# Performance work log

Hardware: AMD Instinct MI355X
Metric: run time of the kernel (lower is better)

## Reference

```python
import jax, jax.numpy as jnp
import numpy as np

N_POINTS = 2097152
FEAT_DIM = 32
RES = [256, 256, 256, 128]  # xyzt resolutions
COO_COMBS = [[0, 3], [1, 3], [2, 3]]
INIT_A, INIT_B = 0.1, 0.5


def _bilinear_sample(plane, cx, cy):
    """F.grid_sample(align_corners=True, padding_mode='border') for one plane.

    plane: [F, H, W]; cx, cy: [N] normalized coords in [-1, 1].
    Returns [N, F].
    """
    Fd, H, W = plane.shape
    # unnormalize (align_corners=True) then border-clamp the coordinate itself
    x = jnp.clip((cx + 1.0) * 0.5 * (W - 1), 0.0, W - 1)
    y = jnp.clip((cy + 1.0) * 0.5 * (H - 1), 0.0, H - 1)
    x0 = jnp.floor(x)
    y0 = jnp.floor(y)
    wx = (x - x0)[:, None]
    wy = (y - y0)[:, None]
    x0i = x0.astype(jnp.int32)
    y0i = y0.astype(jnp.int32)
    x1i = jnp.minimum(x0i + 1, W - 1)
    y1i = jnp.minimum(y0i + 1, H - 1)
    p = jnp.transpose(plane, (1, 2, 0))  # [H, W, F] for gather
    v00 = p[y0i, x0i]  # [N, F]
    v01 = p[y0i, x1i]
    v10 = p[y1i, x0i]
    v11 = p[y1i, x1i]
    return (v00 * (1 - wx) * (1 - wy) + v01 * wx * (1 - wy)
            + v10 * (1 - wx) * wy + v11 * wx * wy)


def setup_inputs() -> dict:
    key = jax.random.key(0)
    k_inp, k0, k1, k2 = jax.random.split(key, 4)
    inp = jax.random.uniform(k_inp, (N_POINTS, 4), dtype=jnp.float32,
                             minval=-1.0, maxval=1.0)
    planes = {}
    for name, k, comb in (("plane0", k0, COO_COMBS[0]),
                          ("plane1", k1, COO_COMBS[1]),
                          ("plane2", k2, COO_COMBS[2])):
        shape = (FEAT_DIM, RES[comb[1]], RES[comb[0]])
        planes[name] = jax.random.uniform(k, shape, dtype=jnp.float32,
                                          minval=INIT_A, maxval=INIT_B)
    return {"inp": inp, **planes}


def reference(inp, plane0, plane1, plane2):
    # reduce='sum': sum of three bilinear plane lookups
    out = 0.0
    for plane, comb in zip((plane0, plane1, plane2), COO_COMBS):
        out = out + _bilinear_sample(plane, inp[..., comb[0]], inp[..., comb[1]])
    return out  # [N, FEAT_DIM]
```

## Files before the change

kernel.cpp:

```cpp
#include <hip/hip_runtime.h>
#include <hip/hip_fp16.h>


#define NPTS 2097152
#define FEAT 32
#define PW 256
#define PH 128
#define NBINS 128
#define BIN_CAP 24576
#define NCHUNKS 4

__global__ __launch_bounds__(128) void zero_counts_kernel(int* counts) {
    counts[threadIdx.x] = 0;
}

__global__ __launch_bounds__(1024) void scatter_kernel(
    const float* __restrict__ inp,
    float4* __restrict__ s_pts,
    int* __restrict__ counts) {
    __shared__ int hist[NBINS];
    __shared__ int base[NBINS];
    int tid = threadIdx.x;
    if (tid < NBINS) hist[tid] = 0;
    __syncthreads();

    float4 c[8];
    int tag[8];
    unsigned int pw[8];
    int p0 = blockIdx.x * 8192 + tid;
#pragma unroll
    for (int i = 0; i < 8; ++i) {
        c[i] = reinterpret_cast<const float4*>(inp)[p0 + i * 1024];
        float y = fminf(fmaxf((c[i].w + 1.0f) * 63.5f, 0.0f), 127.0f);
        float bf = floorf(y);
        int bin = (int)bf;
        int wyq = (int)((y - bf) * 2048.0f);
        pw[i] = ((unsigned int)(p0 + i * 1024) << 11) | (unsigned int)wyq;
        int lpos = atomicAdd(&hist[bin], 1);
        tag[i] = (bin << 16) | lpos;
    }
    __syncthreads();
    if (tid < NBINS) base[tid] = atomicAdd(&counts[tid], hist[tid]);
    __syncthreads();
#pragma unroll
    for (int i = 0; i < 8; ++i) {
        int bin = tag[i] >> 16;
        int pos = base[bin] + (tag[i] & 0xffff);
        s_pts[bin * BIN_CAP + pos] =
            make_float4(c[i].x, c[i].y, c[i].z, __uint_as_float(pw[i]));
    }
}

__device__ __forceinline__ unsigned int pk16(float a, float b) {
    __half2 h = __floats2half2_rn(a, b);
    return *reinterpret_cast<unsigned int*>(&h);
}
__device__ __forceinline__ float2 up16(unsigned int u) {
    __half2 h = *reinterpret_cast<__half2*>(&u);
    return __half22float2(h);
}

__global__ __launch_bounds__(1024) void sample_lds_kernel(
    const float* __restrict__ pl0,
    const float* __restrict__ pl1,
    const float* __restrict__ pl2,
    const float4* __restrict__ s_pts,
    const int* __restrict__ counts,
    float* __restrict__ out) {
    __shared__ uint4 tex[6 * PW * 4];
    __shared__ float bounce[FEAT * PW];

    const int chunk = blockIdx.x;
    const int bin = blockIdx.y;
    const int tid = threadIdx.x;
    const int r1 = min(bin + 1, PH - 1);
    const float* planes[3] = {pl0, pl1, pl2};

    for (int i = 0; i < 6; ++i) {
        const float* src = planes[i >> 1] + ((i & 1) ? r1 : bin) * PW;
        {
            int f = tid >> 6;
            int x4 = (tid & 63) << 2;
            float4 a = *reinterpret_cast<const float4*>(src + f * (PH * PW) + x4);
            float4 b = *reinterpret_cast<const float4*>(src + (f + 16) * (PH * PW) + x4);
            *reinterpret_cast<float4*>(bounce + f * PW + x4) = a;
            *reinterpret_cast<float4*>(bounce + (f + 16) * PW + x4) = b;
        }
        __syncthreads();
        {
            int slot = tid >> 8;
            int x = tid & 255;
            const float* bp = bounce + (slot << 3) * PW + x;
            uint4 v;
            v.x = pk16(bp[0],      bp[PW]);
            v.y = pk16(bp[2 * PW], bp[3 * PW]);
            v.z = pk16(bp[4 * PW], bp[5 * PW]);
            v.w = pk16(bp[6 * PW], bp[7 * PW]);
            int swz = (slot + ((x >> 1) & 3)) & 3;
            tex[(i << 10) | (x << 2) | swz] = v;
        }
        __syncthreads();
    }

    const int cnt = min(counts[bin], BIN_CAP);
    const int pid = tid >> 2;
    const int f4 = tid & 3;

    for (int s0 = chunk * 256; s0 < cnt; s0 += NCHUNKS * 256) {
        int slot = s0 + pid;
        if (slot < cnt) {
            float4 c = s_pts[bin * BIN_CAP + slot];
            unsigned int pw = __float_as_uint(c.w);
            int id = pw >> 11;
            float wy = (float)(pw & 2047u) * (1.0f / 2048.0f);
            float omy = 1.0f - wy;

            float a0 = 0, a1 = 0, a2 = 0, a3 = 0, a4 = 0, a5 = 0, a6 = 0, a7 = 0;
            const float cx[3] = {c.x, c.y, c.z};
#pragma unroll
            for (int k = 0; k < 3; ++k) {
                float x = fminf(fmaxf((cx[k] + 1.0f) * 127.5f, 0.0f), 255.0f);
                float x0f = floorf(x);
                float wx = x - x0f;
                float omx = 1.0f - wx;
                int x0 = (int)x0f;
                int x1 = min(x0 + 1, PW - 1);
                float w00 = omx * omy, w01 = wx * omy;
                float w10 = omx * wy, w11 = wx * wy;

                int b0 = (k * 2) << 10;
                int b1 = b0 + 1024;
                int i0 = (x0 << 2) | ((f4 + ((x0 >> 1) & 3)) & 3);
                int i1 = (x1 << 2) | ((f4 + ((x1 >> 1) & 3)) & 3);
                uint4 t00 = tex[b0 | i0];
                uint4 t01 = tex[b0 | i1];
                uint4 t10 = tex[b1 | i0];
                uint4 t11 = tex[b1 | i1];
#define ACC(T, W) { float2 u0 = up16(T.x), u1 = up16(T.y), u2 = up16(T.z), u3 = up16(T.w); \
                a0 += u0.x * W; a1 += u0.y * W; a2 += u1.x * W; a3 += u1.y * W; \
                a4 += u2.x * W; a5 += u2.y * W; a6 += u3.x * W; a7 += u3.y * W; }
                ACC(t00, w00) ACC(t01, w01) ACC(t10, w10) ACC(t11, w11)
#undef ACC
            }
            float* op = out + ((size_t)id << 5) + (f4 << 3);
            *reinterpret_cast<float4*>(op) = make_float4(a0, a1, a2, a3);
            *reinterpret_cast<float4*>(op + 4) = make_float4(a4, a5, a6, a7);
        }
    }
}

__global__ __launch_bounds__(256) void sample_fallback_kernel(
    const float* __restrict__ inp,
    const float* __restrict__ pl0,
    const float* __restrict__ pl1,
    const float* __restrict__ pl2,
    float* __restrict__ out) {
    int t = blockIdx.x * 256 + threadIdx.x;
    int p = t >> 3;
    int f4 = t & 7;
    float4 c = reinterpret_cast<const float4*>(inp)[p];
    float y = fminf(fmaxf((c.w + 1.0f) * 63.5f, 0.0f), 127.0f);
    float y0f = floorf(y);
    float wy = y - y0f;
    int y0 = (int)y0f;
    int y1 = min(y0 + 1, PH - 1);
    float omy = 1.0f - wy;
    const float* planes[3] = {pl0, pl1, pl2};
    const float cx[3] = {c.x, c.y, c.z};
    float acc[4] = {0.f, 0.f, 0.f, 0.f};
#pragma unroll
    for (int k = 0; k < 3; ++k) {
        float x = fminf(fmaxf((cx[k] + 1.0f) * 127.5f, 0.0f), 255.0f);
        float x0f = floorf(x);
        float wx = x - x0f;
        int x0 = (int)x0f;
        int x1 = min(x0 + 1, PW - 1);
        float omx = 1.0f - wx;
        float w00 = omx * omy, w01 = wx * omy, w10 = omx * wy, w11 = wx * wy;
#pragma unroll
        for (int j = 0; j < 4; ++j) {
            const float* pf = planes[k] + (size_t)(f4 * 4 + j) * (PH * PW);
            acc[j] += pf[y0 * PW + x0] * w00 + pf[y0 * PW + x1] * w01
                    + pf[y1 * PW + x0] * w10 + pf[y1 * PW + x1] * w11;
        }
    }
    *reinterpret_cast<float4*>(out + ((size_t)p << 5) + (f4 << 2)) =
        make_float4(acc[0], acc[1], acc[2], acc[3]);
}

extern "C" void kernel_launch(void* const* d_in, const int* in_sizes, int n_in,
                              void* d_out, int out_size, void* d_ws, size_t ws_size,
                              hipStream_t stream) {
    const float* inp = (const float*)d_in[0];
    const float* pl0 = (const float*)d_in[1];
    const float* pl1 = (const float*)d_in[2];
    const float* pl2 = (const float*)d_in[3];
    float* out = (float*)d_out;

    const size_t pts_bytes = (size_t)NBINS * BIN_CAP * sizeof(float4);
    const size_t need = pts_bytes + NBINS * sizeof(int);

    if (ws_size >= need) {
        float4* s_pts = (float4*)d_ws;
        int* counts = (int*)((char*)d_ws + pts_bytes);

        zero_counts_kernel<<<1, NBINS, 0, stream>>>(counts);
        scatter_kernel<<<NPTS / 8192, 1024, 0, stream>>>(inp, s_pts, counts);
        dim3 grid(NCHUNKS, NBINS);
        sample_lds_kernel<<<grid, 1024, 0, stream>>>(pl0, pl1, pl2, s_pts, counts, out);
    } else {
        sample_fallback_kernel<<<(NPTS * 8) / 256, 256, 0, stream>>>(inp, pl0, pl1, pl2, out);
    }
}
```

Measured before the change: 386.0 us.

## Replace global binning with per-block LDS sort and global fp16 texture

Drops the global scatter into workspace bins and the per-bin LDS texture build. A transpose kernel now packs all three planes into one global fp16 feature-interleaved texture. Each sample block sorts its own 8192 points by row in LDS using a local prefix scan, then gathers from the global texture through cache. This removes the workspace round trip and the global atomics, at the cost of gathers that go through L2/L1 instead of LDS. Input loads and output stores are marked nontemporal.

```diff
diff --git a/kernel.cpp b/kernel.cpp
--- a/kernel.cpp
+++ b/kernel.cpp
@@ -7,49 +7,11 @@
 #define PW 256
 #define PH 128
 #define NBINS 128
-#define BIN_CAP 24576
-#define NCHUNKS 4
+#define PPB 8192
 
-__global__ __launch_bounds__(128) void zero_counts_kernel(int* counts) {
-    counts[threadIdx.x] = 0;
-}
+typedef float fx4 __attribute__((ext_vector_type(4)));
 
-__global__ __launch_bounds__(1024) void scatter_kernel(
-    const float* __restrict__ inp,
-    float4* __restrict__ s_pts,
-    int* __restrict__ counts) {
-    __shared__ int hist[NBINS];
-    __shared__ int base[NBINS];
-    int tid = threadIdx.x;
-    if (tid < NBINS) hist[tid] = 0;
-    __syncthreads();
-
-    float4 c[8];
-    int tag[8];
-    unsigned int pw[8];
-    int p0 = blockIdx.x * 8192 + tid;
-#pragma unroll
-    for (int i = 0; i < 8; ++i) {
-        c[i] = reinterpret_cast<const float4*>(inp)[p0 + i * 1024];
-        float y = fminf(fmaxf((c[i].w + 1.0f) * 63.5f, 0.0f), 127.0f);
-        float bf = floorf(y);
-        int bin = (int)bf;
-        int wyq = (int)((y - bf) * 2048.0f);
-        pw[i] = ((unsigned int)(p0 + i * 1024) << 11) | (unsigned int)wyq;
-        int lpos = atomicAdd(&hist[bin], 1);
-        tag[i] = (bin << 16) | lpos;
-    }
-    __syncthreads();
-    if (tid < NBINS) base[tid] = atomicAdd(&counts[tid], hist[tid]);
-    __syncthreads();
-#pragma unroll
-    for (int i = 0; i < 8; ++i) {
-        int bin = tag[i] >> 16;
-        int pos = base[bin] + (tag[i] & 0xffff);
-        s_pts[bin * BIN_CAP + pos] =
-            make_float4(c[i].x, c[i].y, c[i].z, __uint_as_float(pw[i]));
-    }
-}
+__device__ uint4 g_tex[3 * PH * PW * 4];
 
 __device__ __forceinline__ unsigned int pk16(float a, float b) {
     __half2 h = __floats2half2_rn(a, b);
@@ -60,132 +22,132 @@
     return __half22float2(h);
 }
 
-__global__ __launch_bounds__(1024) void sample_lds_kernel(
-    const float* __restrict__ pl0,
-    const float* __restrict__ pl1,
-    const float* __restrict__ pl2,
-    const float4* __restrict__ s_pts,
-    const int* __restrict__ counts,
+__global__ __launch_bounds__(256) void transpose_kernel(
+    const float* __restrict__ p0,
+    const float* __restrict__ p1,
+    const float* __restrict__ p2) {
+    __shared__ float b[FEAT][PW + 2];
+    const int k = blockIdx.x >> 7;
+    const int y = blockIdx.x & 127;
+    const int tid = threadIdx.x;
+    const float* src = ((k == 0) ? p0 : (k == 1) ? p1 : p2) + y * PW;
+#pragma unroll
+    for (int f = 0; f < FEAT; ++f)
+        b[f][tid] = src[(size_t)f * (PH * PW) + tid];
+    __syncthreads();
+    const int x = tid;
+    uint4 v[4];
+#pragma unroll
+    for (int j = 0; j < 4; ++j) {
+        v[j].x = pk16(b[8 * j + 0][x], b[8 * j + 1][x]);
+        v[j].y = pk16(b[8 * j + 2][x], b[8 * j + 3][x]);
+        v[j].z = pk16(b[8 * j + 4][x], b[8 * j + 5][x]);
+        v[j].w = pk16(b[8 * j + 6][x], b[8 * j + 7][x]);
+    }
+    uint4* dst = g_tex + (size_t)(((k * PH + y) * PW + x)) * 4;
+#pragma unroll
+    for (int j = 0; j < 4; ++j) dst[j] = v[j];
+}
+
+__global__ __launch_bounds__(1024) void sample_kernel(
+    const float* __restrict__ inp,
     float* __restrict__ out) {
-    __shared__ uint4 tex[6 * PW * 4];
-    __shared__ float bounce[FEAT * PW];
+    __shared__ float4 spts[PPB];
+    __shared__ int hist[NBINS];
+    __shared__ int sA[NBINS], sB[NBINS];
 
-    const int chunk = blockIdx.x;
-    const int bin = blockIdx.y;
     const int tid = threadIdx.x;
-    const int r1 = min(bin + 1, PH - 1);
-    const float* planes[3] = {pl0, pl1, pl2};
+    const size_t pbase = (size_t)blockIdx.x * PPB;
 
-    for (int i = 0; i < 6; ++i) {
-        const float* src = planes[i >> 1] + ((i & 1) ? r1 : bin) * PW;
-        {
-            int f = tid >> 6;
-            int x4 = (tid & 63) << 2;
-            float4 a = *reinterpret_cast<const float4*>(src + f * (PH * PW) + x4);
-            float4 b = *reinterpret_cast<const float4*>(src + (f + 16) * (PH * PW) + x4);
-            *reinterpret_cast<float4*>(bounce + f * PW + x4) = a;
-            *reinterpret_cast<float4*>(bounce + (f + 16) * PW + x4) = b;
-        }
-        __syncthreads();
-        {
-            int slot = tid >> 8;
-            int x = tid & 255;
-            const float* bp = bounce + (slot << 3) * PW + x;
-            uint4 v;
-            v.x = pk16(bp[0],      bp[PW]);
-            v.y = pk16(bp[2 * PW], bp[3 * PW]);
-            v.z = pk16(bp[4 * PW], bp[5 * PW]);
-            v.w = pk16(bp[6 * PW], bp[7 * PW]);
-            int swz = (slot + ((x >> 1) & 3)) & 3;
-            tex[(i << 10) | (x << 2) | swz] = v;
+    if (tid < NBINS) hist[tid] = 0;
+    __syncthreads();
+
+    float4 c[8];
+    int tag[8];
+    unsigned int pw[8];
+#pragma unroll
+    for (int i = 0; i < 8; ++i) {
+        int lid = tid + i * 1024;
+        fx4 cv = __builtin_nontemporal_load(
+            reinterpret_cast<const fx4*>(inp) + (pbase + lid));
+        c[i] = make_float4(cv.x, cv.y, cv.z, cv.w);
+        float y = fminf(fmaxf((c[i].w + 1.0f) * 63.5f, 0.0f), 127.0f);
+        float bf = floorf(y);
+        int bin = (int)bf;
+        int wyq = (int)((y - bf) * 2048.0f);
+        pw[i] = ((unsigned int)bin << 24) | ((unsigned int)lid << 11)
+              | (unsigned int)wyq;
+        int lpos = atomicAdd(&hist[bin], 1);
+        tag[i] = (bin << 16) | lpos;
+    }
+    __syncthreads();
+
+    if (tid < NBINS) sA[tid] = hist[tid];
+    __syncthreads();
+#pragma unroll
+    for (int step = 1, s = 0; step < NBINS; step <<= 1, ++s) {
+        if (tid < NBINS) {
+            const int* rd = (s & 1) ? sB : sA;
+            int* wr = (s & 1) ? sA : sB;
+            int v = rd[tid];
+            if (tid >= step) v += rd[tid - step];
+            wr[tid] = v;
         }
         __syncthreads();
     }
+    if (tid < NBINS) sA[tid] = sB[tid] - hist[tid];
+    __syncthreads();
 
-    const int cnt = min(counts[bin], BIN_CAP);
-    const int pid = tid >> 2;
+#pragma unroll
+    for (int i = 0; i < 8; ++i) {
+        int pos = sA[tag[i] >> 16] + (tag[i] & 0xffff);
+        spts[pos] = make_float4(c[i].x, c[i].y, c[i].z, __uint_as_float(pw[i]));
+    }
+    __syncthreads();
+
     const int f4 = tid & 3;
+    const uint4* tex = g_tex;
 
-    for (int s0 = chunk * 256; s0 < cnt; s0 += NCHUNKS * 256) {
-        int slot = s0 + pid;
-        if (slot < cnt) {
-            float4 c = s_pts[bin * BIN_CAP + slot];
-            unsigned int pw = __float_as_uint(c.w);
-            int id = pw >> 11;
-            float wy = (float)(pw & 2047u) * (1.0f / 2048.0f);
-            float omy = 1.0f - wy;
+    for (int it = 0; it < PPB / 256; ++it) {
+        float4 p = spts[it * 256 + (tid >> 2)];
+        unsigned int w = __float_as_uint(p.w);
+        int bin = (int)(w >> 24);
+        int lid = (int)((w >> 11) & 8191u);
+        float wy = (float)(w & 2047u) * (1.0f / 2048.0f);
+        float omy = 1.0f - wy;
+        int y1 = min(bin + 1, PH - 1);
 
-            float a0 = 0, a1 = 0, a2 = 0, a3 = 0, a4 = 0, a5 = 0, a6 = 0, a7 = 0;
-            const float cx[3] = {c.x, c.y, c.z};
+        float a0 = 0, a1 = 0, a2 = 0, a3 = 0, a4 = 0, a5 = 0, a6 = 0, a7 = 0;
+        const float cx[3] = {p.x, p.y, p.z};
 #pragma unroll
-            for (int k = 0; k < 3; ++k) {
-                float x = fminf(fmaxf((cx[k] + 1.0f) * 127.5f, 0.0f), 255.0f);
-                float x0f = floorf(x);
-                float wx = x - x0f;
-                float omx = 1.0f - wx;
-                int x0 = (int)x0f;
-                int x1 = min(x0 + 1, PW - 1);
-                float w00 = omx * omy, w01 = wx * omy;
-                float w10 = omx * wy, w11 = wx * wy;
+        for (int k = 0; k < 3; ++k) {
+            float x = fminf(fmaxf((cx[k] + 1.0f) * 127.5f, 0.0f), 255.0f);
+            float x0f = floorf(x);
+            float wx = x - x0f;
+            float omx = 1.0f - wx;
+            int x0 = (int)x0f;
+            int x1 = min(x0 + 1, PW - 1);
+            float w00 = omx * omy, w01 = wx * omy;
+            float w10 = omx * wy, w11 = wx * wy;
 
-                int b0 = (k * 2) << 10;
-                int b1 = b0 + 1024;
-                int i0 = (x0 << 2) | ((f4 + ((x0 >> 1) & 3)) & 3);
-                int i1 = (x1 << 2) | ((f4 + ((x1 >> 1) & 3)) & 3);
-                uint4 t00 = tex[b0 | i0];
-                uint4 t01 = tex[b0 | i1];
-                uint4 t10 = tex[b1 | i0];
-                uint4 t11 = tex[b1 | i1];
+            int rb0 = (k * PH + bin) * PW;
+            int rb1 = (k * PH + y1) * PW;
+            uint4 t00 = tex[((rb0 + x0) << 2) | f4];
+            uint4 t01 = tex[((rb0 + x1) << 2) | f4];
+            uint4 t10 = tex[((rb1 + x0) << 2) | f4];
+            uint4 t11 = tex[((rb1 + x1) << 2) | f4];
 #define ACC(T, W) { float2 u0 = up16(T.x), u1 = up16(T.y), u2 = up16(T.z), u3 = up16(T.w); \
-                a0 += u0.x * W; a1 += u0.y * W; a2 += u1.x * W; a3 += u1.y * W; \
-                a4 += u2.x * W; a5 += u2.y * W; a6 += u3.x * W; a7 += u3.y * W; }
-                ACC(t00, w00) ACC(t01, w01) ACC(t10, w10) ACC(t11, w11)
+            a0 += u0.x * W; a1 += u0.y * W; a2 += u1.x * W; a3 += u1.y * W; \
+            a4 += u2.x * W; a5 += u2.y * W; a6 += u3.x * W; a7 += u3.y * W; }
+            ACC(t00, w00) ACC(t01, w01) ACC(t10, w10) ACC(t11, w11)
 #undef ACC
-            }
-            float* op = out + ((size_t)id << 5) + (f4 << 3);
-            *reinterpret_cast<float4*>(op) = make_float4(a0, a1, a2, a3);
-            *reinterpret_cast<float4*>(op + 4) = make_float4(a4, a5, a6, a7);
         }
+        float* op = out + ((pbase + (size_t)lid) << 5) + (f4 << 3);
+        fx4 o0 = {a0, a1, a2, a3};
+        fx4 o1 = {a4, a5, a6, a7};
+        __builtin_nontemporal_store(o0, reinterpret_cast<fx4*>(op));
+        __builtin_nontemporal_store(o1, reinterpret_cast<fx4*>(op + 4));
     }
-}
-
-__global__ __launch_bounds__(256) void sample_fallback_kernel(
-    const float* __restrict__ inp,
-    const float* __restrict__ pl0,
-    const float* __restrict__ pl1,
-    const float* __restrict__ pl2,
-    float* __restrict__ out) {
-    int t = blockIdx.x * 256 + threadIdx.x;
-    int p = t >> 3;
-    int f4 = t & 7;
-    float4 c = reinterpret_cast<const float4*>(inp)[p];
-    float y = fminf(fmaxf((c.w + 1.0f) * 63.5f, 0.0f), 127.0f);
-    float y0f = floorf(y);
-    float wy = y - y0f;
-    int y0 = (int)y0f;
-    int y1 = min(y0 + 1, PH - 1);
-    float omy = 1.0f - wy;
-    const float* planes[3] = {pl0, pl1, pl2};
-    const float cx[3] = {c.x, c.y, c.z};
-    float acc[4] = {0.f, 0.f, 0.f, 0.f};
-#pragma unroll
-    for (int k = 0; k < 3; ++k) {
-        float x = fminf(fmaxf((cx[k] + 1.0f) * 127.5f, 0.0f), 255.0f);
-        float x0f = floorf(x);
-        float wx = x - x0f;
-        int x0 = (int)x0f;
-        int x1 = min(x0 + 1, PW - 1);
-        float omx = 1.0f - wx;
-        float w00 = omx * omy, w01 = wx * omy, w10 = omx * wy, w11 = wx * wy;
-#pragma unroll
-        for (int j = 0; j < 4; ++j) {
-            const float* pf = planes[k] + (size_t)(f4 * 4 + j) * (PH * PW);
-            acc[j] += pf[y0 * PW + x0] * w00 + pf[y0 * PW + x1] * w01
-                    + pf[y1 * PW + x0] * w10 + pf[y1 * PW + x1] * w11;
-        }
-    }
-    *reinterpret_cast<float4*>(out + ((size_t)p << 5) + (f4 << 2)) =
-        make_float4(acc[0], acc[1], acc[2], acc[3]);
 }
 
 extern "C" void kernel_launch(void* const* d_in, const int* in_sizes, int n_in,
@@ -196,19 +158,8 @@
     const float* pl1 = (const float*)d_in[2];
     const float* pl2 = (const float*)d_in[3];
     float* out = (float*)d_out;
+    (void)d_ws; (void)ws_size;
 
-    const size_t pts_bytes = (size_t)NBINS * BIN_CAP * sizeof(float4);
-    const size_t need = pts_bytes + NBINS * sizeof(int);
-
-    if (ws_size >= need) {
-        float4* s_pts = (float4*)d_ws;
-        int* counts = (int*)((char*)d_ws + pts_bytes);
-
-        zero_counts_kernel<<<1, NBINS, 0, stream>>>(counts);
-        scatter_kernel<<<NPTS / 8192, 1024, 0, stream>>>(inp, s_pts, counts);
-        dim3 grid(NCHUNKS, NBINS);
-        sample_lds_kernel<<<grid, 1024, 0, stream>>>(pl0, pl1, pl2, s_pts, counts, out);
-    } else {
-        sample_fallback_kernel<<<(NPTS * 8) / 256, 256, 0, stream>>>(inp, pl0, pl1, pl2, out);
-    }
+    transpose_kernel<<<3 * PH, 256, 0, stream>>>(pl0, pl1, pl2);
+    sample_kernel<<<NPTS / PPB, 1024, 0, stream>>>(inp, out);
 }
```

Result: slower. 395.6 us (+2.5%).
